# Kernel tuning notes

Measured on AMD Instinct MI355X. Metric: run time of the kernel, lower is better.

## Reference

```python
import jax, jax.numpy as jnp
import numpy as np

BIG = 2 ** 30  # sentinel label for background / padding


def _shift(a, dy, dx):
    # Shift last-two-dims image by (dy, dx), filling with BIG.
    H, W = a.shape[-2], a.shape[-1]
    pad = [(0, 0)] * (a.ndim - 2) + [(max(dy, 0), max(-dy, 0)), (max(dx, 0), max(-dx, 0))]
    ap = jnp.pad(a, pad, constant_values=BIG)
    ys, xs = max(-dy, 0), max(-dx, 0)
    return ap[..., ys:ys + H, xs:xs + W]


def _cc_counts(fg):
    # fg: bool [..., H, W]. Returns int32 [...] = number of 4-connected components
    # per image (== reduce_max of tfa.image.connected_components labels).
    H, W = fg.shape[-2], fg.shape[-1]
    idx = jnp.arange(H * W, dtype=jnp.int32).reshape(H, W)
    init = jnp.where(fg, idx, BIG)

    def step(lbl):
        nbr = jnp.minimum(jnp.minimum(_shift(lbl, 1, 0), _shift(lbl, -1, 0)),
                          jnp.minimum(_shift(lbl, 0, 1), _shift(lbl, 0, -1)))
        return jnp.where(fg, jnp.minimum(lbl, nbr), BIG)

    def cond(c):
        prev, cur = c
        return jnp.any(prev != cur)

    def body(c):
        _, cur = c
        return (cur, step(cur))

    _, final = jax.lax.while_loop(cond, body, (init, step(init)))
    # Each component's minimum-index pixel keeps its initial label -> one root per component.
    roots = fg & (final == init)
    return jnp.sum(roots.astype(jnp.int32), axis=(-2, -1))


def setup_inputs() -> dict:
    key = jax.random.key(0)
    # [n_color, n_box, batch, patches, H, W] binary images as float 0/1
    x = jax.random.randint(key, (2, 2, 8, 64, 64, 64), 0, 2).astype(jnp.float32)
    return {"x": x}


def reference(x) -> jnp.ndarray:
    fg = x > 0.5  # [C, B, batch, patches, H, W] boolean
    counts = _cc_counts(fg)  # [C, B, batch, patches] int32 component counts
    n_patches = counts.shape[-1]
    # tf.reduce_mean on int tensors truncates (integer division), then cast.
    mean_i = jnp.sum(counts, axis=-1) // n_patches  # [C, B, batch]
    return mean_i.astype(jnp.float32)
```

## Files before the change

kernel.cpp:

```cpp
#include <hip/hip_runtime.h>

constexpr int NPIX = 64 * 64;
constexpr int PATCHES = 64;
constexpr int RUNS_PER_ROW = 32;
constexpr int TABLE = 64 * RUNS_PER_ROW;

__device__ __forceinline__ int find_root(volatile int* p, int i) {
    while (true) {
        int pi = p[i];
        if (pi == i) return i;
        int gp = p[pi];
        if (gp == pi) return pi;
        p[i] = gp;
        i = gp;
    }
}

__device__ __forceinline__ int merge(int* p, int a, int b) {
    while (true) {
        a = find_root(p, a);
        b = find_root(p, b);
        if (a == b) return 0;
        if (a > b) { int t = a; a = b; b = t; }
        int old = atomicMin(&p[b], a);
        if (old == b) return 1;
        b = old;
    }
}

__global__ __launch_bounds__(256, 8) void cc_kernel(const float* __restrict__ in,
                                                    int* __restrict__ counts) {
    __shared__ int par[TABLE];
    __shared__ unsigned long long mrow[64];
    __shared__ int wpart[4];
    const int tid = threadIdx.x;
    const int img = blockIdx.x;
    const int r = tid >> 2;
    const int q = tid & 3;

    const float4* src =
        reinterpret_cast<const float4*>(in + (size_t)img * NPIX + r * 64 + q * 16);
    float4 buf[4];
#pragma unroll
    for (int k = 0; k < 4; ++k) buf[k] = src[k];

    {
        int b0 = tid * 4;
        *reinterpret_cast<int4*>(&par[b0]) = make_int4(b0, b0 + 1, b0 + 2, b0 + 3);
        int b1 = 1024 + tid * 4;
        *reinterpret_cast<int4*>(&par[b1]) = make_int4(b1, b1 + 1, b1 + 2, b1 + 3);
    }

    unsigned qm = 0;
#pragma unroll
    for (int k = 0; k < 4; ++k) {
        qm |= (buf[k].x > 0.5f ? 1u : 0u) << (4 * k);
        qm |= (buf[k].y > 0.5f ? 2u : 0u) << (4 * k);
        qm |= (buf[k].z > 0.5f ? 4u : 0u) << (4 * k);
        qm |= (buf[k].w > 0.5f ? 8u : 0u) << (4 * k);
    }
    unsigned long long m = (unsigned long long)qm << (16 * q);
    m |= __shfl_xor(m, 1, 4);
    m |= __shfl_xor(m, 2, 4);

    if (q == 0) mrow[r] = m;
    __syncthreads();

    const unsigned long long ma = m;
    const unsigned long long mb = (r < 63) ? mrow[r + 1] : 0ull;
    const unsigned long long sa = ma & ~(ma << 1);
    const unsigned long long sb = mb & ~(mb << 1);
    const unsigned long long qmask = 0xFFFFull << (16 * q);

    int cnt = __popcll(sa & qmask);

    unsigned long long both = ma & mb;
    unsigned long long ov = (both & ~(both << 1)) & qmask;
    while (ov) {
        int x = __builtin_ctzll(ov);
        ov &= ov - 1;
        unsigned long long below = (2ull << x) - 1;
        int ida = r * RUNS_PER_ROW + __popcll(sa & below) - 1;
        int idb = (r + 1) * RUNS_PER_ROW + __popcll(sb & below) - 1;
        cnt -= merge(par, ida, idb);
    }

#pragma unroll
    for (int d = 32; d > 0; d >>= 1) cnt += __shfl_xor(cnt, d, 64);
    if ((tid & 63) == 0) wpart[tid >> 6] = cnt;
    __syncthreads();
    if (tid == 0) counts[img] = wpart[0] + wpart[1] + wpart[2] + wpart[3];
}

__global__ void finalize_kernel(const int* __restrict__ counts,
                                float* __restrict__ out, int ngroups) {
    const int t = threadIdx.x;
    const int g = t >> 3, j = t & 7;
    if (g >= ngroups) return;
    const int* c = counts + g * PATCHES + j * 8;
    int s = 0;
#pragma unroll
    for (int k = 0; k < 8; ++k) s += c[k];
#pragma unroll
    for (int d = 4; d > 0; d >>= 1) s += __shfl_down(s, d, 8);
    if (j == 0) out[g] = (float)(s >> 6);
}

extern "C" void kernel_launch(void* const* d_in, const int* in_sizes, int n_in,
                              void* d_out, int out_size, void* d_ws, size_t ws_size,
                              hipStream_t stream) {
    const float* x = (const float*)d_in[0];
    float* out = (float*)d_out;
    int* counts = (int*)d_ws;

    const int nimg = in_sizes[0] / NPIX;
    const int ngroups = out_size;

    cc_kernel<<<nimg, 256, 0, stream>>>(x, counts);
    finalize_kernel<<<1, ngroups * 8, 0, stream>>>(counts, out, ngroups);
}
```

Measured before the change: 21.34 us.

## Compact merge pairs into per-wave worklist and use lock-free Rem-style union

Each thread's overlapping run pairs are compacted through a wave prefix scan into a shared-memory worklist. The wave then processes that list with all lanes busy, removing the imbalance where lanes with several overlaps serialize the loop. find_root plus merge is replaced by a Rem-style splicing merge that uses atomicMin on parent links. The cost is an extra scan, a shared buffer that lowers occupancy headroom, and a block barrier.

Measured after the change: 23.80 us. +11.5%, slower.

```diff
diff --git a/kernel.cpp b/kernel.cpp
--- a/kernel.cpp
+++ b/kernel.cpp
@@ -4,39 +4,37 @@
 constexpr int PATCHES = 64;
 constexpr int RUNS_PER_ROW = 32;
 constexpr int TABLE = 64 * RUNS_PER_ROW;
+constexpr int WL_PER_WAVE = 512;
 
-__device__ __forceinline__ int find_root(volatile int* p, int i) {
-    while (true) {
-        int pi = p[i];
-        if (pi == i) return i;
-        int gp = p[pi];
-        if (gp == pi) return pi;
-        p[i] = gp;
-        i = gp;
+__device__ __forceinline__ int merge(int* p, int x, int y) {
+    int px = p[x], py = p[y];
+    while (px != py) {
+        if (px < py) { int t = x; x = y; y = t; t = px; px = py; py = t; }
+        if (px == x) {
+            int old = atomicMin(&p[x], py);
+            if (old == x) return 1;
+            px = old;
+        } else {
+            atomicMin(&p[x], py);
+            x = px;
+            px = p[x];
+        }
     }
-}
-
-__device__ __forceinline__ int merge(int* p, int a, int b) {
-    while (true) {
-        a = find_root(p, a);
-        b = find_root(p, b);
-        if (a == b) return 0;
-        if (a > b) { int t = a; a = b; b = t; }
-        int old = atomicMin(&p[b], a);
-        if (old == b) return 1;
-        b = old;
-    }
+    return 0;
 }
 
 __global__ __launch_bounds__(256, 8) void cc_kernel(const float* __restrict__ in,
                                                     int* __restrict__ counts) {
     __shared__ int par[TABLE];
     __shared__ unsigned long long mrow[64];
+    __shared__ unsigned wl[4][WL_PER_WAVE];
     __shared__ int wpart[4];
     const int tid = threadIdx.x;
     const int img = blockIdx.x;
     const int r = tid >> 2;
     const int q = tid & 3;
+    const int wid = tid >> 6;
+    const int lane = tid & 63;
 
     const float4* src =
         reinterpret_cast<const float4*>(in + (size_t)img * NPIX + r * 64 + q * 16);
@@ -76,18 +74,35 @@
 
     unsigned long long both = ma & mb;
     unsigned long long ov = (both & ~(both << 1)) & qmask;
+    const int nseg = __popcll(ov);
+
+    int pre = nseg;
+#pragma unroll
+    for (int d = 1; d < 64; d <<= 1) {
+        int t = __shfl_up(pre, d, 64);
+        if (lane >= d) pre += t;
+    }
+    const int wtotal = __shfl(pre, 63, 64);
+    int idx = pre - nseg;
+
     while (ov) {
         int x = __builtin_ctzll(ov);
         ov &= ov - 1;
         unsigned long long below = (2ull << x) - 1;
         int ida = r * RUNS_PER_ROW + __popcll(sa & below) - 1;
         int idb = (r + 1) * RUNS_PER_ROW + __popcll(sb & below) - 1;
-        cnt -= merge(par, ida, idb);
+        wl[wid][idx++] = ((unsigned)ida << 11) | (unsigned)idb;
+    }
+    __syncthreads();
+
+    for (int t = lane; t < wtotal; t += 64) {
+        unsigned pr = wl[wid][t];
+        cnt -= merge(par, (int)(pr >> 11), (int)(pr & 2047u));
     }
 
 #pragma unroll
     for (int d = 32; d > 0; d >>= 1) cnt += __shfl_xor(cnt, d, 64);
-    if ((tid & 63) == 0) wpart[tid >> 6] = cnt;
+    if (lane == 0) wpart[wid] = cnt;
     __syncthreads();
     if (tid == 0) counts[img] = wpart[0] + wpart[1] + wpart[2] + wpart[3];
 }
```

## Split union-find merges into even/odd row phases and simplify root finding

Applied to the files above, without the earlier changes.

Merges between adjacent row pairs now run in two phases: even rows first, then odd rows after a barrier. The first phase merges disjoint row pairs, which cuts atomic contention and gives shallow trees before the second phase. Root finding now walks both chains together with no path compression. This trades shorter, more parallel find loops for possibly longer chains and an extra barrier, and leaves half of the threads idle in each phase.

After: 22.12 us. 3.6% more time.

```diff
diff --git a/kernel.cpp b/kernel.cpp
--- a/kernel.cpp
+++ b/kernel.cpp
@@ -2,24 +2,19 @@
 
 constexpr int NPIX = 64 * 64;
 constexpr int PATCHES = 64;
-constexpr int RUNS_PER_ROW = 32;
-constexpr int TABLE = 64 * RUNS_PER_ROW;
-
-__device__ __forceinline__ int find_root(volatile int* p, int i) {
-    while (true) {
-        int pi = p[i];
-        if (pi == i) return i;
-        int gp = p[pi];
-        if (gp == pi) return pi;
-        p[i] = gp;
-        i = gp;
-    }
-}
+constexpr int RPR = 32;
+constexpr int TABLE = 64 * RPR;
 
 __device__ __forceinline__ int merge(int* p, int a, int b) {
+    volatile int* vp = p;
     while (true) {
-        a = find_root(p, a);
-        b = find_root(p, b);
+        int pa = vp[a], pb = vp[b];
+        while (pa != a || pb != b) {
+            a = pa;
+            b = pb;
+            pa = vp[a];
+            pb = vp[b];
+        }
         if (a == b) return 0;
         if (a > b) { int t = a; a = b; b = t; }
         int old = atomicMin(&p[b], a);
@@ -76,13 +71,30 @@
 
     unsigned long long both = ma & mb;
     unsigned long long ov = (both & ~(both << 1)) & qmask;
-    while (ov) {
-        int x = __builtin_ctzll(ov);
-        ov &= ov - 1;
-        unsigned long long below = (2ull << x) - 1;
-        int ida = r * RUNS_PER_ROW + __popcll(sa & below) - 1;
-        int idb = (r + 1) * RUNS_PER_ROW + __popcll(sb & below) - 1;
-        cnt -= merge(par, ida, idb);
+
+    if ((r & 1) == 0) {
+        unsigned long long o = ov;
+        while (o) {
+            int x = __builtin_ctzll(o);
+            o &= o - 1;
+            unsigned long long below = (2ull << x) - 1;
+            int ida = r * RPR + __popcll(sa & below) - 1;
+            int idb = (r + 1) * RPR + __popcll(sb & below) - 1;
+            cnt -= merge(par, ida, idb);
+        }
+    }
+    __syncthreads();
+
+    if ((r & 1) == 1) {
+        unsigned long long o = ov;
+        while (o) {
+            int x = __builtin_ctzll(o);
+            o &= o - 1;
+            unsigned long long below = (2ull << x) - 1;
+            int ida = r * RPR + __popcll(sa & below) - 1;
+            int idb = (r + 1) * RPR + __popcll(sb & below) - 1;
+            cnt -= merge(par, ida, idb);
+        }
     }
 
 #pragma unroll
```
